# Performance work log

Hardware: AMD Instinct MI355X
Metric: run time of the kernel (lower is better)

The kernel has to match this reference:

```python
import jax, jax.numpy as jnp
import numpy as np

B, S, D, H = 2, 2048, 1024, 16
DK = D // H


def setup_inputs() -> dict:
    key = jax.random.key(0)
    ks = jax.random.split(key, 7)
    x = jax.random.normal(ks[0], (B, S, D), dtype=jnp.float32)
    gamma = jax.random.normal(ks[1], (D,), dtype=jnp.float32)
    mask = jax.random.randint(ks[2], (B, S), 0, 2, dtype=jnp.int32)
    w_qkv_w = jax.random.normal(ks[3], (D, 3 * D), dtype=jnp.float32) / np.sqrt(D)
    w_qkv_b = jax.random.normal(ks[4], (3 * D,), dtype=jnp.float32) * 0.02
    w_o_w = jax.random.normal(ks[5], (D, D), dtype=jnp.float32) / np.sqrt(D)
    w_o_b = jax.random.normal(ks[6], (D,), dtype=jnp.float32) * 0.02
    return {"x": x, "gamma": gamma, "mask": mask, "w_qkv_w": w_qkv_w,
            "w_qkv_b": w_qkv_b, "w_o_w": w_o_w, "w_o_b": w_o_b}


def reference(x, gamma, mask, w_qkv_w, w_qkv_b, w_o_w, w_o_b):
    b, s, d = x.shape
    # QKV projection, then per-head interleaved chunk (matches torch view+chunk)
    qkv = x @ w_qkv_w + w_qkv_b                      # [B,S,3D]
    qkv = qkv.reshape(b, s, H, 3 * DK).transpose(0, 2, 1, 3)  # [B,H,S,3*dk]
    q, k, v = jnp.split(qkv, 3, axis=-1)             # each [B,H,S,dk]
    scale = 1.0 / np.sqrt(DK).astype(np.float32)
    scores = jnp.einsum('bhqd,bhkd->bhqk', q, k) * scale  # [B,H,S,S]
    m = mask[:, None, None, :]                       # 2D mask -> [B,1,1,S]
    scores = jnp.where(m == 0, -jnp.inf, scores)
    attn = jax.nn.softmax(scores, axis=-1)           # dropout p=0.0 -> identity
    out = jnp.einsum('bhqk,bhkd->bhqd', attn, v)     # [B,H,S,dk]
    out = out.transpose(0, 2, 1, 3).reshape(b, s, d) # [B,S,D]
    out = out @ w_o_w + w_o_b
    return (gamma + 1.0) * out
```

## Files before the change

kernel.cpp:

```cpp
#include <hip/hip_runtime.h>
#include <hip/hip_bf16.h>


using bf16 = __hip_bfloat16;
typedef __attribute__((ext_vector_type(8))) short bf16x8;
typedef __attribute__((ext_vector_type(4))) float f32x4;

#define QSCALE 0.18033688011112042f

static __device__ __forceinline__ f32x4 mfma_bf16(bf16x8 a, bf16x8 b, f32x4 c) {
    return __builtin_amdgcn_mfma_f32_16x16x32_bf16(a, b, c, 0, 0, 0);
}

static __device__ __forceinline__ void gld_lds16(const void* g, void* s) {
    __builtin_amdgcn_global_load_lds(
        (const __attribute__((address_space(1))) unsigned int*)g,
        (__attribute__((address_space(3))) unsigned int*)s,
        16, 0, 0);
}

static __device__ __forceinline__ short f2s(float f) {
    bf16 h = __float2bfloat16(f);
    return *reinterpret_cast<short*>(&h);
}

__global__ void prep_kernel(const float* __restrict__ x, bf16* __restrict__ xb,
                            const float* __restrict__ wqkv, bf16* __restrict__ wqkvT,
                            const float* __restrict__ wo, bf16* __restrict__ woT) {
    __shared__ float tile[32][33];
    int blk = blockIdx.x;
    if (blk < 4096) {
        int i = blk * 256 + threadIdx.x;
        float4 f = reinterpret_cast<const float4*>(x)[i];
        xb[4*i+0] = __float2bfloat16(f.x);
        xb[4*i+1] = __float2bfloat16(f.y);
        xb[4*i+2] = __float2bfloat16(f.z);
        xb[4*i+3] = __float2bfloat16(f.w);
        return;
    }
    const float* in; bf16* out; int R, C, bx, by;
    if (blk < 7168) {
        int idx = blk - 4096; in = wqkv; out = wqkvT; R = 1024; C = 3072;
        bx = idx % 96; by = idx / 96;
    } else {
        int idx = blk - 7168; in = wo; out = woT; R = 1024; C = 1024;
        bx = idx & 31; by = idx >> 5;
    }
    int c0 = bx * 32, r0 = by * 32;
    int xo = threadIdx.x & 31, yo = threadIdx.x >> 5;
#pragma unroll
    for (int i = 0; i < 32; i += 8) tile[yo + i][xo] = in[(size_t)(r0 + yo + i) * C + c0 + xo];
    __syncthreads();
#pragma unroll
    for (int i = 0; i < 32; i += 8)
        out[(size_t)(c0 + yo + i) * R + r0 + xo] = __float2bfloat16(tile[xo][yo + i]);
}

__global__ void transpose_v_kernel(const bf16* __restrict__ in, bf16* __restrict__ out) {
    __shared__ bf16 t[64][72];
    const int bh = blockIdx.y, s0 = blockIdx.x * 64;
    const int r = threadIdx.x >> 2, c16 = (threadIdx.x & 3) * 16;
    const uint4* src = (const uint4*)(in + ((size_t)bh * 2048 + s0 + r) * 64 + c16);
    uint4 a0 = src[0], a1 = src[1];
    *(uint4*)&t[r][c16] = a0;
    *(uint4*)&t[r][c16 + 8] = a1;
    __syncthreads();
    bf16 tmp[16];
#pragma unroll
    for (int ii = 0; ii < 16; ++ii) {
        int i = c16 + ii;
        int a = i >> 5, rem = i & 31, q = rem >> 3, jj = rem & 7;
        int sp = a * 32 + q * 4 + (jj < 4 ? jj : 16 + jj - 4);
        tmp[ii] = t[sp][r];
    }
    uint4* dst = (uint4*)(out + ((size_t)bh * 64 + r) * 2048 + s0 + c16);
    dst[0] = ((uint4*)tmp)[0];
    dst[1] = ((uint4*)tmp)[1];
}

template <int EPI, int TM, int MINW>
__global__ __launch_bounds__(256, MINW)
void gemm_bt_kernel(const bf16* __restrict__ A, const bf16* __restrict__ Bt,
                    int M, int N, int K,
                    const float* __restrict__ bias, const float* __restrict__ gamma,
                    bf16* __restrict__ Qout, bf16* __restrict__ Kout, bf16* __restrict__ Vout,
                    float* __restrict__ Cout) {
    constexpr int MI = TM / 32;
    constexpr int CA = TM / 32;
    __shared__ __align__(16) bf16 As[TM * 64];
    __shared__ __align__(16) bf16 Bs[128 * 64];

    const int tid  = threadIdx.x;
    const int wave = tid >> 6, lane = tid & 63;
    const int quad = lane >> 4, l16 = lane & 15;
    const int wr = wave >> 1, wc = wave & 1;
    const int bm = blockIdx.y, bn = blockIdx.x;

    f32x4 acc[MI][4] = {};

    const int crow = lane >> 3;
    const int sblk = (lane & 7) ^ (crow & 7);
    const bf16* gA[CA]; const bf16* gB[4]; bf16* lA[CA]; bf16* lB[4];
#pragma unroll
    for (int c = 0; c < CA; ++c) {
        int ch = wave * CA + c;
        gA[c] = A + (size_t)(bm * TM + ch * 8 + crow) * K + sblk * 8;
        lA[c] = As + ch * 512 + lane * 8;
    }
#pragma unroll
    for (int c = 0; c < 4; ++c) {
        int ch = wave * 4 + c;
        gB[c] = Bt + (size_t)(bn * 128 + ch * 8 + crow) * K + sblk * 8;
        lB[c] = Bs + ch * 512 + lane * 8;
    }
    const int xr = l16 & 7;

    for (int k0 = 0; k0 < K; k0 += 64) {
#pragma unroll
        for (int c = 0; c < CA; ++c) gld_lds16(gA[c] + k0, lA[c]);
#pragma unroll
        for (int c = 0; c < 4; ++c) gld_lds16(gB[c] + k0, lB[c]);
        __syncthreads();
#pragma unroll
        for (int ks = 0; ks < 2; ++ks) {
            bf16x8 af[MI], bfr[4];
#pragma unroll
            for (int mi = 0; mi < MI; ++mi)
                af[mi] = *(const bf16x8*)(As + (wr * (TM/2) + mi * 16 + l16) * 64 + ((4 * ks + quad) ^ xr) * 8);
#pragma unroll
            for (int ni = 0; ni < 4; ++ni)
                bfr[ni] = *(const bf16x8*)(Bs + (wc * 64 + ni * 16 + l16) * 64 + ((4 * ks + quad) ^ xr) * 8);
#pragma unroll
            for (int mi = 0; mi < MI; ++mi)
#pragma unroll
                for (int ni = 0; ni < 4; ++ni)
                    acc[mi][ni] = mfma_bf16(af[mi], bfr[ni], acc[mi][ni]);
        }
        __syncthreads();
    }

#pragma unroll
    for (int mi = 0; mi < MI; ++mi) {
#pragma unroll
        for (int ni = 0; ni < 4; ++ni) {
#pragma unroll
            for (int r = 0; r < 4; ++r) {
                int row = bm * TM + wr * (TM/2) + mi * 16 + quad * 4 + r;
                int col = bn * 128 + wc * 64 + ni * 16 + l16;
                float v = acc[mi][ni][r];
                if (EPI == 0) {
                    v += bias[col];
                    int h = col / 192;
                    int rr = col - h * 192;
                    int which = rr >> 6, dk = rr & 63;
                    int b = row >> 11, s = row & 2047;
                    size_t bh = (size_t)b * 16 + h;
                    if (which == 0) {
                        Qout[(bh * 2048 + s) * 64 + dk] = __float2bfloat16(v * QSCALE);
                    } else if (which == 1) {
                        Kout[(bh * 2048 + s) * 64 + dk] = __float2bfloat16(v);
                    } else {
                        Vout[(bh * 2048 + s) * 64 + dk] = __float2bfloat16(v);
                    }
                } else {
                    float o = (gamma[col] + 1.0f) * (v + bias[col]);
                    Cout[(size_t)row * N + col] = o;
                }
            }
        }
    }
}

__global__ __launch_bounds__(256, 2)
void attn_kernel(const bf16* __restrict__ Qb, const bf16* __restrict__ Kb,
                 const bf16* __restrict__ Vtp, const int* __restrict__ mask,
                 bf16* __restrict__ Aout) {
    __shared__ __align__(16) bf16 Ks[2][64 * 64];
    __shared__ __align__(16) bf16 Vs[2][64 * 64];
    __shared__ float Biass[2][64];

    const int lid = blockIdx.x + (blockIdx.y << 4);
    const int w   = (lid & 7) * 64 + (lid >> 3);
    const int bh  = w >> 4;
    const int b = bh >> 4, h = bh & 15;
    const int q0 = (w & 15) * 128;
    const int tid = threadIdx.x;
    const int wave = tid >> 6, lane = tid & 63;
    const int quad = lane >> 4, l16 = lane & 15;
    const int xr = l16 & 7;

    bf16x8 aq[2][2];
#pragma unroll
    for (int m = 0; m < 2; ++m) {
        const bf16* qp = Qb + ((size_t)bh * 2048 + q0 + wave * 32 + m * 16 + l16) * 64;
        aq[m][0] = *(const bf16x8*)(qp + quad * 8);
        aq[m][1] = *(const bf16x8*)(qp + 32 + quad * 8);
    }

    bf16x8 ones;
#pragma unroll
    for (int j = 0; j < 8; ++j) ones[j] = (short)0x3F80;

    f32x4 O[2][4] = {};
    f32x4 Lacc[2] = {};

    const int r8 = lane >> 3, b8 = lane & 7;
    const int srcb = b8 ^ r8;
    const bf16* gK = Kb  + ((size_t)bh * 2048 + wave * 8 + r8) * 64 + srcb * 8;
    const bf16* gV = Vtp + ((size_t)bh * 64 + wave * 8 + r8) * 2048 + srcb * 8;
    bf16* lK[2][2]; bf16* lV[2][2];
#pragma unroll
    for (int p = 0; p < 2; ++p)
#pragma unroll
        for (int c = 0; c < 2; ++c) {
            lK[p][c] = Ks[p] + c * 2048 + wave * 512 + lane * 8;
            lV[p][c] = Vs[p] + c * 2048 + wave * 512 + lane * 8;
        }

    int mreg = 0;
#pragma unroll
    for (int c = 0; c < 2; ++c) {
        gld_lds16(gK + c * 2048, lK[0][c]);
        gld_lds16(gV + (size_t)c * 65536, lV[0][c]);
    }
    if (tid < 64) {
        Biass[0][tid] = mask[b * 2048 + tid] ? -24.0f : -1e30f;
        mreg = mask[b * 2048 + 64 + tid];
    }

    for (int kt = 0; kt < 32; ++kt) {
        __syncthreads();
        const int cur = kt & 1, nxt = cur ^ 1;

        if (kt + 1 < 32) {
#pragma unroll
            for (int c = 0; c < 2; ++c) {
                gld_lds16(gK + (size_t)(kt + 1) * 4096 + c * 2048, lK[nxt][c]);
                gld_lds16(gV + (kt + 1) * 64 + (size_t)c * 65536, lV[nxt][c]);
            }
            if (tid < 64) Biass[nxt][tid] = mreg ? -24.0f : -1e30f;
        }
        if (kt + 2 < 32 && tid < 64) mreg = mask[b * 2048 + (kt + 2) * 64 + tid];

        f32x4 bias4[4];
        bf16x8 bk[4][2];
#pragma unroll
        for (int kt4 = 0; kt4 < 4; ++kt4) {
            bias4[kt4] = *(const f32x4*)(&Biass[cur][0] + kt4 * 16 + quad * 4);
            const bf16* kp = Ks[cur] + (kt4 * 16 + l16) * 64;
            bk[kt4][0] = *(const bf16x8*)(kp + (quad ^ xr) * 8);
            bk[kt4][1] = *(const bf16x8*)(kp + ((quad + 4) ^ xr) * 8);
        }
        bf16x8 bv8[2][4];
#pragma unroll
        for (int a = 0; a < 2; ++a)
#pragma unroll
            for (int nt = 0; nt < 4; ++nt)
                bv8[a][nt] = *(const bf16x8*)(Vs[cur] + (nt * 16 + l16) * 64 + ((a * 4 + quad) ^ xr) * 8);

        f32x4 sv[2][4];
        __builtin_amdgcn_s_setprio(1);
#pragma unroll
        for (int m = 0; m < 2; ++m)
#pragma unroll
            for (int kt4 = 0; kt4 < 4; ++kt4) {
                f32x4 c = mfma_bf16(bk[kt4][0], aq[m][0], bias4[kt4]);
                sv[m][kt4] = mfma_bf16(bk[kt4][1], aq[m][1], c);
            }
        __builtin_amdgcn_s_setprio(0);

        float p[2][4][4];
#pragma unroll
        for (int m = 0; m < 2; ++m)
#pragma unroll
            for (int kt4 = 0; kt4 < 4; ++kt4)
#pragma unroll
                for (int r = 0; r < 4; ++r)
                    p[m][kt4][r] = __builtin_amdgcn_exp2f(sv[m][kt4][r]);

#pragma unroll
        for (int m = 0; m < 2; ++m) {
#pragma unroll
            for (int a = 0; a < 2; ++a) {
                bf16x8 pa;
                pa[0] = f2s(p[m][2*a][0]);   pa[1] = f2s(p[m][2*a][1]);
                pa[2] = f2s(p[m][2*a][2]);   pa[3] = f2s(p[m][2*a][3]);
                pa[4] = f2s(p[m][2*a+1][0]); pa[5] = f2s(p[m][2*a+1][1]);
                pa[6] = f2s(p[m][2*a+1][2]); pa[7] = f2s(p[m][2*a+1][3]);
                __builtin_amdgcn_s_setprio(1);
                Lacc[m] = mfma_bf16(pa, ones, Lacc[m]);
#pragma unroll
                for (int nt = 0; nt < 4; ++nt)
                    O[m][nt] = mfma_bf16(pa, bv8[a][nt], O[m][nt]);
                __builtin_amdgcn_s_setprio(0);
            }
        }
    }

#pragma unroll
    for (int m = 0; m < 2; ++m) {
        float inv[4];
#pragma unroll
        for (int r = 0; r < 4; ++r) inv[r] = __builtin_amdgcn_rcpf(Lacc[m][r]);
#pragma unroll
        for (int nt = 0; nt < 4; ++nt) {
#pragma unroll
            for (int r = 0; r < 4; ++r) {
                int row = q0 + wave * 32 + m * 16 + quad * 4 + r;
                Aout[((size_t)b * 2048 + row) * 1024 + h * 64 + nt * 16 + l16] =
                    __float2bfloat16(O[m][nt][r] * inv[r]);
            }
        }
    }
}

extern "C" void kernel_launch(void* const* d_in, const int* in_sizes, int n_in,
                              void* d_out, int out_size, void* d_ws, size_t ws_size,
                              hipStream_t stream) {
    const float* x     = (const float*)d_in[0];
    const float* gamma = (const float*)d_in[1];
    const int*   mask  = (const int*)d_in[2];
    const float* wqkv  = (const float*)d_in[3];
    const float* bqkv  = (const float*)d_in[4];
    const float* wo    = (const float*)d_in[5];
    const float* bo    = (const float*)d_in[6];
    float* out = (float*)d_out;

    char* ws = (char*)d_ws;
    const size_t MB = 1u << 20;
    bf16* xb    = (bf16*)(ws);
    bf16* wqkvT = (bf16*)(ws + 8 * MB);
    bf16* woT   = (bf16*)(ws + 14 * MB);
    bf16* Qb    = (bf16*)(ws + 16 * MB);
    bf16* Kb    = (bf16*)(ws + 24 * MB);
    bf16* Vt    = (bf16*)(ws + 32 * MB);
    bf16* Vtmp  = (bf16*)(ws + 40 * MB);
    bf16* attn  = (bf16*)(ws + 40 * MB);

    prep_kernel<<<8192, 256, 0, stream>>>(x, xb, wqkv, wqkvT, wo, woT);

    gemm_bt_kernel<0, 128, 3><<<dim3(24, 32), 256, 0, stream>>>(
        xb, wqkvT, 4096, 3072, 1024, bqkv, nullptr, Qb, Kb, Vtmp, nullptr);

    transpose_v_kernel<<<dim3(32, 32), 256, 0, stream>>>(Vtmp, Vt);

    attn_kernel<<<dim3(16, 32), 256, 0, stream>>>(Qb, Kb, Vt, mask, attn);

    gemm_bt_kernel<1, 64, 4><<<dim3(8, 64), 256, 0, stream>>>(
        attn, woT, 4096, 1024, 1024, bo, gamma, nullptr, nullptr, nullptr, out);
}
```

Before: 192.0 us.

## Load K/V tiles directly from global into registers, dropping LDS staging

The attention kernel no longer stages K, V and the mask bias through double-buffered shared memory with barriers. Each wave now loads its K/V MFMA operands and mask values straight from global memory into registers, prefetching the next tile while the current one is computed. This removes the per-iteration __syncthreads and the LDS traffic. In exchange, the four waves of a block each fetch the same K/V tiles from global/L2, with less coalesced 16-byte loads and higher register pressure.

```diff
diff --git a/kernel.cpp b/kernel.cpp
--- a/kernel.cpp
+++ b/kernel.cpp
@@ -175,10 +175,6 @@
 void attn_kernel(const bf16* __restrict__ Qb, const bf16* __restrict__ Kb,
                  const bf16* __restrict__ Vtp, const int* __restrict__ mask,
                  bf16* __restrict__ Aout) {
-    __shared__ __align__(16) bf16 Ks[2][64 * 64];
-    __shared__ __align__(16) bf16 Vs[2][64 * 64];
-    __shared__ float Biass[2][64];
-
     const int lid = blockIdx.x + (blockIdx.y << 4);
     const int w   = (lid & 7) * 64 + (lid >> 3);
     const int bh  = w >> 4;
@@ -187,7 +183,6 @@
     const int tid = threadIdx.x;
     const int wave = tid >> 6, lane = tid & 63;
     const int quad = lane >> 4, l16 = lane & 15;
-    const int xr = l16 & 7;
 
     bf16x8 aq[2][2];
 #pragma unroll
@@ -204,59 +199,38 @@
     f32x4 O[2][4] = {};
     f32x4 Lacc[2] = {};
 
-    const int r8 = lane >> 3, b8 = lane & 7;
-    const int srcb = b8 ^ r8;
-    const bf16* gK = Kb  + ((size_t)bh * 2048 + wave * 8 + r8) * 64 + srcb * 8;
-    const bf16* gV = Vtp + ((size_t)bh * 64 + wave * 8 + r8) * 2048 + srcb * 8;
-    bf16* lK[2][2]; bf16* lV[2][2];
-#pragma unroll
-    for (int p = 0; p < 2; ++p)
-#pragma unroll
-        for (int c = 0; c < 2; ++c) {
-            lK[p][c] = Ks[p] + c * 2048 + wave * 512 + lane * 8;
-            lV[p][c] = Vs[p] + c * 2048 + wave * 512 + lane * 8;
-        }
-
-    int mreg = 0;
-#pragma unroll
-    for (int c = 0; c < 2; ++c) {
-        gld_lds16(gK + c * 2048, lK[0][c]);
-        gld_lds16(gV + (size_t)c * 65536, lV[0][c]);
-    }
-    if (tid < 64) {
-        Biass[0][tid] = mask[b * 2048 + tid] ? -24.0f : -1e30f;
-        mreg = mask[b * 2048 + 64 + tid];
-    }
+    const bf16* kp = Kb  + ((size_t)bh * 2048 + l16) * 64 + quad * 8;
+    const bf16* vp = Vtp + (size_t)bh * 131072 + (size_t)l16 * 2048 + quad * 8;
+    const int*  mp = mask + b * 2048 + quad * 4;
+
+    bf16x8 bk[4][2], bv[2][4];
+    int4 mi4[4];
+#pragma unroll
+    for (int kt4 = 0; kt4 < 4; ++kt4) {
+        bk[kt4][0] = *(const bf16x8*)(kp + kt4 * 1024);
+        bk[kt4][1] = *(const bf16x8*)(kp + kt4 * 1024 + 32);
+        mi4[kt4]   = *(const int4*)(mp + kt4 * 16);
+    }
+#pragma unroll
+    for (int a = 0; a < 2; ++a)
+#pragma unroll
+        for (int nt = 0; nt < 4; ++nt)
+            bv[a][nt] = *(const bf16x8*)(vp + nt * 32768 + a * 32);
 
     for (int kt = 0; kt < 32; ++kt) {
-        __syncthreads();
-        const int cur = kt & 1, nxt = cur ^ 1;
-
-        if (kt + 1 < 32) {
-#pragma unroll
-            for (int c = 0; c < 2; ++c) {
-                gld_lds16(gK + (size_t)(kt + 1) * 4096 + c * 2048, lK[nxt][c]);
-                gld_lds16(gV + (kt + 1) * 64 + (size_t)c * 65536, lV[nxt][c]);
-            }
-            if (tid < 64) Biass[nxt][tid] = mreg ? -24.0f : -1e30f;
-        }
-        if (kt + 2 < 32 && tid < 64) mreg = mask[b * 2048 + (kt + 2) * 64 + tid];
+        const int ktn = (kt < 31) ? kt + 1 : 31;
+        const bf16* kpn = kp + (size_t)ktn * 4096;
+        const bf16* vpn = vp + ktn * 64;
+        const int*  mpn = mp + ktn * 64;
 
         f32x4 bias4[4];
-        bf16x8 bk[4][2];
 #pragma unroll
         for (int kt4 = 0; kt4 < 4; ++kt4) {
-            bias4[kt4] = *(const f32x4*)(&Biass[cur][0] + kt4 * 16 + quad * 4);
-            const bf16* kp = Ks[cur] + (kt4 * 16 + l16) * 64;
-            bk[kt4][0] = *(const bf16x8*)(kp + (quad ^ xr) * 8);
-            bk[kt4][1] = *(const bf16x8*)(kp + ((quad + 4) ^ xr) * 8);
-        }
-        bf16x8 bv8[2][4];
-#pragma unroll
-        for (int a = 0; a < 2; ++a)
-#pragma unroll
-            for (int nt = 0; nt < 4; ++nt)
-                bv8[a][nt] = *(const bf16x8*)(Vs[cur] + (nt * 16 + l16) * 64 + ((a * 4 + quad) ^ xr) * 8);
+            bias4[kt4][0] = mi4[kt4].x ? -24.0f : -1e30f;
+            bias4[kt4][1] = mi4[kt4].y ? -24.0f : -1e30f;
+            bias4[kt4][2] = mi4[kt4].z ? -24.0f : -1e30f;
+            bias4[kt4][3] = mi4[kt4].w ? -24.0f : -1e30f;
+        }
 
         f32x4 sv[2][4];
         __builtin_amdgcn_s_setprio(1);
@@ -269,32 +243,44 @@
             }
         __builtin_amdgcn_s_setprio(0);
 
-        float p[2][4][4];
+#pragma unroll
+        for (int kt4 = 0; kt4 < 4; ++kt4) {
+            bk[kt4][0] = *(const bf16x8*)(kpn + kt4 * 1024);
+            bk[kt4][1] = *(const bf16x8*)(kpn + kt4 * 1024 + 32);
+            mi4[kt4]   = *(const int4*)(mpn + kt4 * 16);
+        }
+
 #pragma unroll
         for (int m = 0; m < 2; ++m)
 #pragma unroll
             for (int kt4 = 0; kt4 < 4; ++kt4)
 #pragma unroll
                 for (int r = 0; r < 4; ++r)
-                    p[m][kt4][r] = __builtin_amdgcn_exp2f(sv[m][kt4][r]);
+                    sv[m][kt4][r] = __builtin_amdgcn_exp2f(sv[m][kt4][r]);
 
 #pragma unroll
         for (int m = 0; m < 2; ++m) {
 #pragma unroll
             for (int a = 0; a < 2; ++a) {
                 bf16x8 pa;
-                pa[0] = f2s(p[m][2*a][0]);   pa[1] = f2s(p[m][2*a][1]);
-                pa[2] = f2s(p[m][2*a][2]);   pa[3] = f2s(p[m][2*a][3]);
-                pa[4] = f2s(p[m][2*a+1][0]); pa[5] = f2s(p[m][2*a+1][1]);
-                pa[6] = f2s(p[m][2*a+1][2]); pa[7] = f2s(p[m][2*a+1][3]);
+                pa[0] = f2s(sv[m][2*a][0]);   pa[1] = f2s(sv[m][2*a][1]);
+                pa[2] = f2s(sv[m][2*a][2]);   pa[3] = f2s(sv[m][2*a][3]);
+                pa[4] = f2s(sv[m][2*a+1][0]); pa[5] = f2s(sv[m][2*a+1][1]);
+                pa[6] = f2s(sv[m][2*a+1][2]); pa[7] = f2s(sv[m][2*a+1][3]);
                 __builtin_amdgcn_s_setprio(1);
                 Lacc[m] = mfma_bf16(pa, ones, Lacc[m]);
 #pragma unroll
                 for (int nt = 0; nt < 4; ++nt)
-                    O[m][nt] = mfma_bf16(pa, bv8[a][nt], O[m][nt]);
+                    O[m][nt] = mfma_bf16(pa, bv[a][nt], O[m][nt]);
                 __builtin_amdgcn_s_setprio(0);
             }
         }
+
+#pragma unroll
+        for (int a = 0; a < 2; ++a)
+#pragma unroll
+            for (int nt = 0; nt < 4; ++nt)
+                bv[a][nt] = *(const bf16x8*)(vpn + nt * 32768 + a * 32);
     }
 
 #pragma unroll
```

Result: slower. 267.0 us (+39.1%).

## Split attention waves into query and key groups with LDS reduction

Applied to the files above, without the earlier changes.

Each block now loads two 64-key tiles per iteration and splits its four waves into two query groups and two key groups. Each wave handles 64 query rows against half of the keys, so every K/V fragment read from LDS is reused across twice as many queries. The two key-group partial outputs and row sums are combined through LDS at the end. This halves the number of barrier iterations and raises the reuse of K/V LDS reads per wave. In exchange it doubles the accumulator registers, which may hurt occupancy under the 2-blocks launch bound, and it adds an LDS reduction epilogue.

```diff
diff --git a/kernel.cpp b/kernel.cpp
--- a/kernel.cpp
+++ b/kernel.cpp
@@ -175,9 +175,9 @@
 void attn_kernel(const bf16* __restrict__ Qb, const bf16* __restrict__ Kb,
                  const bf16* __restrict__ Vtp, const int* __restrict__ mask,
                  bf16* __restrict__ Aout) {
-    __shared__ __align__(16) bf16 Ks[2][64 * 64];
-    __shared__ __align__(16) bf16 Vs[2][64 * 64];
-    __shared__ float Biass[2][64];
+    __shared__ __align__(16) bf16 Ks[2][2][4096];
+    __shared__ __align__(16) bf16 Vs[2][2][4096];
+    __shared__ float Biass[2][2][64];
 
     const int lid = blockIdx.x + (blockIdx.y << 4);
     const int w   = (lid & 7) * 64 + (lid >> 3);
@@ -186,13 +186,14 @@
     const int q0 = (w & 15) * 128;
     const int tid = threadIdx.x;
     const int wave = tid >> 6, lane = tid & 63;
+    const int qg = wave >> 1, kg = wave & 1;
     const int quad = lane >> 4, l16 = lane & 15;
     const int xr = l16 & 7;
 
-    bf16x8 aq[2][2];
-#pragma unroll
-    for (int m = 0; m < 2; ++m) {
-        const bf16* qp = Qb + ((size_t)bh * 2048 + q0 + wave * 32 + m * 16 + l16) * 64;
+    bf16x8 aq[4][2];
+#pragma unroll
+    for (int m = 0; m < 4; ++m) {
+        const bf16* qp = Qb + ((size_t)bh * 2048 + q0 + qg * 64 + m * 16 + l16) * 64;
         aq[m][0] = *(const bf16x8*)(qp + quad * 8);
         aq[m][1] = *(const bf16x8*)(qp + 32 + quad * 8);
     }
@@ -201,115 +202,138 @@
 #pragma unroll
     for (int j = 0; j < 8; ++j) ones[j] = (short)0x3F80;
 
-    f32x4 O[2][4] = {};
-    f32x4 Lacc[2] = {};
+    f32x4 O[4][4] = {};
+    f32x4 Lacc[4] = {};
 
     const int r8 = lane >> 3, b8 = lane & 7;
     const int srcb = b8 ^ r8;
     const bf16* gK = Kb  + ((size_t)bh * 2048 + wave * 8 + r8) * 64 + srcb * 8;
     const bf16* gV = Vtp + ((size_t)bh * 64 + wave * 8 + r8) * 2048 + srcb * 8;
-    bf16* lK[2][2]; bf16* lV[2][2];
-#pragma unroll
-    for (int p = 0; p < 2; ++p)
+    const int so = wave * 512 + lane * 8;
+
+    int mreg = 0;
+#pragma unroll
+    for (int ti = 0; ti < 2; ++ti)
 #pragma unroll
         for (int c = 0; c < 2; ++c) {
-            lK[p][c] = Ks[p] + c * 2048 + wave * 512 + lane * 8;
-            lV[p][c] = Vs[p] + c * 2048 + wave * 512 + lane * 8;
-        }
-
-    int mreg = 0;
-#pragma unroll
-    for (int c = 0; c < 2; ++c) {
-        gld_lds16(gK + c * 2048, lK[0][c]);
-        gld_lds16(gV + (size_t)c * 65536, lV[0][c]);
-    }
-    if (tid < 64) {
-        Biass[0][tid] = mask[b * 2048 + tid] ? -24.0f : -1e30f;
-        mreg = mask[b * 2048 + 64 + tid];
-    }
-
-    for (int kt = 0; kt < 32; ++kt) {
+            gld_lds16(gK + (size_t)ti * 4096 + c * 2048, &Ks[0][ti][c * 2048 + so]);
+            gld_lds16(gV + (size_t)ti * 64 + c * 65536, &Vs[0][ti][c * 2048 + so]);
+        }
+    if (tid < 128) {
+        Biass[0][tid >> 6][tid & 63] = mask[b * 2048 + tid] ? -24.0f : -1e30f;
+        mreg = mask[b * 2048 + 128 + tid];
+    }
+
+    for (int t = 0; t < 16; ++t) {
         __syncthreads();
-        const int cur = kt & 1, nxt = cur ^ 1;
-
-        if (kt + 1 < 32) {
-#pragma unroll
-            for (int c = 0; c < 2; ++c) {
-                gld_lds16(gK + (size_t)(kt + 1) * 4096 + c * 2048, lK[nxt][c]);
-                gld_lds16(gV + (kt + 1) * 64 + (size_t)c * 65536, lV[nxt][c]);
-            }
-            if (tid < 64) Biass[nxt][tid] = mreg ? -24.0f : -1e30f;
-        }
-        if (kt + 2 < 32 && tid < 64) mreg = mask[b * 2048 + (kt + 2) * 64 + tid];
-
+        const int cur = t & 1, nxt = cur ^ 1;
+
+        if (t < 15) {
+            const int u0 = 2 * t + 2;
+#pragma unroll
+            for (int ti = 0; ti < 2; ++ti)
+#pragma unroll
+                for (int c = 0; c < 2; ++c) {
+                    gld_lds16(gK + (size_t)(u0 + ti) * 4096 + c * 2048, &Ks[nxt][ti][c * 2048 + so]);
+                    gld_lds16(gV + (size_t)(u0 + ti) * 64 + c * 65536, &Vs[nxt][ti][c * 2048 + so]);
+                }
+            if (tid < 128) Biass[nxt][tid >> 6][tid & 63] = mreg ? -24.0f : -1e30f;
+        }
+        if (t < 14 && tid < 128) mreg = mask[b * 2048 + t * 128 + 256 + tid];
+
+        const bf16* kb = &Ks[cur][kg][0];
+        const bf16* vb = &Vs[cur][kg][0];
         f32x4 bias4[4];
         bf16x8 bk[4][2];
 #pragma unroll
         for (int kt4 = 0; kt4 < 4; ++kt4) {
-            bias4[kt4] = *(const f32x4*)(&Biass[cur][0] + kt4 * 16 + quad * 4);
-            const bf16* kp = Ks[cur] + (kt4 * 16 + l16) * 64;
-            bk[kt4][0] = *(const bf16x8*)(kp + (quad ^ xr) * 8);
-            bk[kt4][1] = *(const bf16x8*)(kp + ((quad + 4) ^ xr) * 8);
-        }
-        bf16x8 bv8[2][4];
+            bias4[kt4] = *(const f32x4*)(&Biass[cur][kg][0] + kt4 * 16 + quad * 4);
+            const bf16* kp2 = kb + (kt4 * 16 + l16) * 64;
+            bk[kt4][0] = *(const bf16x8*)(kp2 + (quad ^ xr) * 8);
+            bk[kt4][1] = *(const bf16x8*)(kp2 + ((quad + 4) ^ xr) * 8);
+        }
+        bf16x8 bv[2][4];
 #pragma unroll
         for (int a = 0; a < 2; ++a)
 #pragma unroll
             for (int nt = 0; nt < 4; ++nt)
-                bv8[a][nt] = *(const bf16x8*)(Vs[cur] + (nt * 16 + l16) * 64 + ((a * 4 + quad) ^ xr) * 8);
-
-        f32x4 sv[2][4];
-        __builtin_amdgcn_s_setprio(1);
-#pragma unroll
-        for (int m = 0; m < 2; ++m)
-#pragma unroll
-            for (int kt4 = 0; kt4 < 4; ++kt4) {
-                f32x4 c = mfma_bf16(bk[kt4][0], aq[m][0], bias4[kt4]);
-                sv[m][kt4] = mfma_bf16(bk[kt4][1], aq[m][1], c);
+                bv[a][nt] = *(const bf16x8*)(vb + (nt * 16 + l16) * 64 + ((a * 4 + quad) ^ xr) * 8);
+
+#pragma unroll
+        for (int mp = 0; mp < 2; ++mp) {
+            f32x4 sv[2][4];
+            __builtin_amdgcn_s_setprio(1);
+#pragma unroll
+            for (int mm = 0; mm < 2; ++mm)
+#pragma unroll
+                for (int kt4 = 0; kt4 < 4; ++kt4) {
+                    f32x4 c = mfma_bf16(bk[kt4][0], aq[mp * 2 + mm][0], bias4[kt4]);
+                    sv[mm][kt4] = mfma_bf16(bk[kt4][1], aq[mp * 2 + mm][1], c);
+                }
+            __builtin_amdgcn_s_setprio(0);
+
+#pragma unroll
+            for (int mm = 0; mm < 2; ++mm)
+#pragma unroll
+                for (int kt4 = 0; kt4 < 4; ++kt4)
+#pragma unroll
+                    for (int r = 0; r < 4; ++r)
+                        sv[mm][kt4][r] = __builtin_amdgcn_exp2f(sv[mm][kt4][r]);
+
+#pragma unroll
+            for (int mm = 0; mm < 2; ++mm) {
+                const int m = mp * 2 + mm;
+#pragma unroll
+                for (int a = 0; a < 2; ++a) {
+                    bf16x8 pa;
+                    pa[0] = f2s(sv[mm][2*a][0]);   pa[1] = f2s(sv[mm][2*a][1]);
+                    pa[2] = f2s(sv[mm][2*a][2]);   pa[3] = f2s(sv[mm][2*a][3]);
+                    pa[4] = f2s(sv[mm][2*a+1][0]); pa[5] = f2s(sv[mm][2*a+1][1]);
+                    pa[6] = f2s(sv[mm][2*a+1][2]); pa[7] = f2s(sv[mm][2*a+1][3]);
+                    __builtin_amdgcn_s_setprio(1);
+                    Lacc[m] = mfma_bf16(pa, ones, Lacc[m]);
+#pragma unroll
+                    for (int nt = 0; nt < 4; ++nt)
+                        O[m][nt] = mfma_bf16(pa, bv[a][nt], O[m][nt]);
+                    __builtin_amdgcn_s_setprio(0);
+                }
             }
-        __builtin_amdgcn_s_setprio(0);
-
-        float p[2][4][4];
-#pragma unroll
-        for (int m = 0; m < 2; ++m)
-#pragma unroll
-            for (int kt4 = 0; kt4 < 4; ++kt4)
+        }
+    }
+
+    __syncthreads();
+    float* cb = (float*)&Ks[0][0][0];
+    float* lb = (float*)&Vs[0][0][0];
+    if (kg == 1) {
+#pragma unroll
+        for (int m = 0; m < 4; ++m) {
+#pragma unroll
+            for (int nt = 0; nt < 4; ++nt)
 #pragma unroll
                 for (int r = 0; r < 4; ++r)
-                    p[m][kt4][r] = __builtin_amdgcn_exp2f(sv[m][kt4][r]);
-
-#pragma unroll
-        for (int m = 0; m < 2; ++m) {
-#pragma unroll
-            for (int a = 0; a < 2; ++a) {
-                bf16x8 pa;
-                pa[0] = f2s(p[m][2*a][0]);   pa[1] = f2s(p[m][2*a][1]);
-                pa[2] = f2s(p[m][2*a][2]);   pa[3] = f2s(p[m][2*a][3]);
-                pa[4] = f2s(p[m][2*a+1][0]); pa[5] = f2s(p[m][2*a+1][1]);
-                pa[6] = f2s(p[m][2*a+1][2]); pa[7] = f2s(p[m][2*a+1][3]);
-                __builtin_amdgcn_s_setprio(1);
-                Lacc[m] = mfma_bf16(pa, ones, Lacc[m]);
-#pragma unroll
-                for (int nt = 0; nt < 4; ++nt)
-                    O[m][nt] = mfma_bf16(pa, bv8[a][nt], O[m][nt]);
-                __builtin_amdgcn_s_setprio(0);
-            }
-        }
-    }
-
-#pragma unroll
-    for (int m = 0; m < 2; ++m) {
-        float inv[4];
-#pragma unroll
-        for (int r = 0; r < 4; ++r) inv[r] = __builtin_amdgcn_rcpf(Lacc[m][r]);
-#pragma unroll
-        for (int nt = 0; nt < 4; ++nt) {
-#pragma unroll
-            for (int r = 0; r < 4; ++r) {
-                int row = q0 + wave * 32 + m * 16 + quad * 4 + r;
-                Aout[((size_t)b * 2048 + row) * 1024 + h * 64 + nt * 16 + l16] =
-                    __float2bfloat16(O[m][nt][r] * inv[r]);
-            }
+                    cb[qg * 4096 + (m * 16 + nt * 4 + r) * 64 + lane] = O[m][nt][r];
+#pragma unroll
+            for (int r = 0; r < 4; ++r)
+                lb[qg * 1024 + (m * 4 + r) * 64 + lane] = Lacc[m][r];
+        }
+    }
+    __syncthreads();
+    if (kg == 0) {
+#pragma unroll
+        for (int m = 0; m < 4; ++m) {
+            float inv[4];
+#pragma unroll
+            for (int r = 0; r < 4; ++r)
+                inv[r] = __builtin_amdgcn_rcpf(Lacc[m][r] + lb[qg * 1024 + (m * 4 + r) * 64 + lane]);
+#pragma unroll
+            for (int nt = 0; nt < 4; ++nt)
+#pragma unroll
+                for (int r = 0; r < 4; ++r) {
+                    int row = q0 + qg * 64 + m * 16 + quad * 4 + r;
+                    float o = O[m][nt][r] + cb[qg * 4096 + (m * 16 + nt * 4 + r) * 64 + lane];
+                    Aout[((size_t)b * 2048 + row) * 1024 + h * 64 + nt * 16 + l16] =
+                        __float2bfloat16(o * inv[r]);
+                }
         }
     }
 }
```

New measurement: 183.8 us. -4.2%, faster.
